# Optimization experiments

Measured on AMD Instinct MI355X. Metric: run time of the kernel, lower is better.

The kernel has to match this reference:

```python
import jax, jax.numpy as jnp
import numpy as np

EPS = 1e-8
NUM_HEADS = 8


def setup_inputs() -> dict:
    key = jax.random.key(0)
    ks = jax.random.split(key, 12)
    B, T, F = 8, 512, 512
    H = NUM_HEADS
    dh = F // H
    maxlen = 2048
    s = 0.02  # weight init scale
    inp = {
        "x": jax.random.normal(ks[0], (B, T, F), jnp.float32),
        "Wq": jax.random.normal(ks[1], (F, F), jnp.float32) * s,
        "bq": jax.random.normal(ks[2], (F,), jnp.float32) * s,
        "Wk": jax.random.normal(ks[3], (F, F), jnp.float32) * s,
        "bk": jax.random.normal(ks[4], (F,), jnp.float32) * s,
        "Wv": jax.random.normal(ks[5], (F, F), jnp.float32) * s,
        "bv": jax.random.normal(ks[6], (F,), jnp.float32) * s,
        "Wo": jax.random.normal(ks[7], (F, F), jnp.float32) * s,
        "bo": jax.random.normal(ks[8], (F,), jnp.float32) * s,
        "delta": jnp.ones((1,), jnp.float32),
        "cache_k": jax.random.normal(ks[9], (B * H, maxlen, dh), jnp.float32) * 0.1,
        "cache_v": jax.random.normal(ks[10], (B * H, maxlen, dh), jnp.float32) * 0.1,
    }
    return inp


def _split_heads(t, H):
    # torch.cat(torch.split(t, dh, dim=-1), dim=0): head index outermost on dim 0
    B, T, F = t.shape
    dh = F // H
    return t.reshape(B, T, H, dh).transpose(2, 0, 1, 3).reshape(H * B, T, dh)


def _merge_heads(t, H):
    HB, T, dh = t.shape
    B = HB // H
    return t.reshape(H, B, T, dh).transpose(1, 2, 0, 3).reshape(B, T, H * dh)


def reference(x, Wq, bq, Wk, bk, Wv, bv, Wo, bo, delta, cache_k, cache_v):
    B, T, F = x.shape
    H = NUM_HEADS
    maxlen = cache_k.shape[1]
    d = jnp.sqrt(jnp.asarray(F, jnp.float32))

    q = _split_heads(x @ Wq.T + bq, H)  # [H*B, T, dh]
    k = _split_heads(x @ Wk.T + bk, H)
    v = _split_heads(x @ Wv.T + bv, H)

    # rolling KV cache: drop oldest T, append new T -> length maxlen
    k_full = jnp.concatenate([cache_k[:, T:], k], axis=1)  # [H*B, maxlen, dh]
    v_full = jnp.concatenate([cache_v[:, T:], v], axis=1)

    # Gaussian positional bias G = exp(-(i-j)^2 / (delta^2 + EPS)), last T rows
    i = jnp.arange(maxlen, dtype=jnp.float32)
    ind = -(i[:, None] - i[None, :]) ** 2  # [maxlen, maxlen]
    G = jnp.exp(ind[-T:] / (delta[0] ** 2 + EPS))  # [T, maxlen]

    scores = jnp.abs(jnp.einsum('btd,bsd->bts', q, k_full) * G / d)
    attn = jax.nn.softmax(scores, axis=-1)  # [H*B, T, maxlen]
    o = jnp.einsum('bts,bsd->btd', attn, v_full)  # [H*B, T, dh]

    out = _merge_heads(o, H) @ Wo.T + bo  # [B, T, F]
    return out
```

## Files before the change

### kernel.cpp

```cpp
#include <hip/hip_runtime.h>
#include <cstdint>
#include <cstddef>


typedef _Float16 f16x8 __attribute__((ext_vector_type(8)));
typedef _Float16 f16x4 __attribute__((ext_vector_type(4)));
typedef float f32x4 __attribute__((ext_vector_type(4)));

#define GLOBAL_AS __attribute__((address_space(1)))
#define LDS_AS __attribute__((address_space(3)))

__launch_bounds__(256)
__global__ void prep(const float* __restrict__ x,
                     const float* __restrict__ Wq, const float* __restrict__ Wk,
                     const float* __restrict__ Wv, const float* __restrict__ Wo,
                     const float* __restrict__ cache_v,
                     _Float16* __restrict__ xh, _Float16* __restrict__ wh,
                     float* __restrict__ part, float* __restrict__ svnew) {
  const int bid = blockIdx.x;
  const int tid = threadIdx.x;
  if (bid < 2048) {
    long e = ((long)bid * 256 + tid) * 4;
    float4 v = *(const float4*)(x + e);
    f16x4 h;
    h[0] = (_Float16)v.x; h[1] = (_Float16)v.y;
    h[2] = (_Float16)v.z; h[3] = (_Float16)v.w;
    *(f16x4*)(xh + e) = h;
  } else if (bid < 3072) {
    long e = ((long)(bid - 2048) * 256 + tid) * 4;
    int seg = (int)(e >> 18);
    const float* w = seg == 0 ? Wq : seg == 1 ? Wk : seg == 2 ? Wv : Wo;
    float4 v = *(const float4*)(w + (e & 262143));
    f16x4 h;
    h[0] = (_Float16)v.x; h[1] = (_Float16)v.y;
    h[2] = (_Float16)v.z; h[3] = (_Float16)v.w;
    *(f16x4*)(wh + e) = h;
  } else if (bid < 4096) {
    int pb = bid - 3072;
    int hb = pb >> 4, chunk = pb & 15;
    int d = tid & 63, p = tid >> 6;
    int r0 = 512 + chunk * 96;
    float s = 0.f;
    for (int r = r0 + p; r < r0 + 96; r += 4)
      s += cache_v[((size_t)hb * 2048 + r) * 64 + d];
    __shared__ float red[256];
    red[tid] = s;
    __syncthreads();
    if (p == 0)
      part[(hb * 16 + chunk) * 64 + d] =
          red[d] + red[64 + d] + red[128 + d] + red[192 + d];
  } else {
    for (int i = tid; i < 4096; i += 256) svnew[i] = 0.f;
  }
}

__launch_bounds__(256)
__global__ void gemm_qkv(const _Float16* __restrict__ xh,
                         const _Float16* __restrict__ wh,
                         const float* __restrict__ bq,
                         const float* __restrict__ bk,
                         const float* __restrict__ bv,
                         _Float16* __restrict__ q, _Float16* __restrict__ k,
                         _Float16* __restrict__ v,
                         float* __restrict__ svnew) {
  __shared__ __align__(16) _Float16 As[2 * 128 * 32];
  __shared__ __align__(16) _Float16 Bs[2 * 64 * 32];
  const int tid = threadIdx.x;
  const int m0 = blockIdx.x * 128;
  const int n0g = blockIdx.y * 64;
  const int which = n0g >> 9;
  const int nloc0 = n0g & 511;
  const _Float16* Bsel = wh + (size_t)which * 262144;
  const float* bsel = which == 0 ? bq : which == 1 ? bk : bv;
  _Float16* osel = which == 0 ? q : which == 1 ? k : v;
  const int w = tid >> 6, lane = tid & 63;
  const int c16 = lane & 15, q4 = lane >> 4;
  const int wm = (w & 1) * 64, wn = (w >> 1) * 32;

  f32x4 acc[4][2];
#pragma unroll
  for (int i = 0; i < 4; i++)
#pragma unroll
    for (int j = 0; j < 2; j++) acc[i][j] = (f32x4){0.f, 0.f, 0.f, 0.f};

  for (int k0 = 0; k0 < 512; k0 += 64) {
    __syncthreads();
#pragma unroll
    for (int it = 0; it < 4; it++) {
      int c = it * 256 + tid;
      int sub = c >> 9, row = (c >> 2) & 127, c8 = (c & 3) * 8;
      __builtin_amdgcn_global_load_lds(
          (const GLOBAL_AS void*)(xh + (size_t)(m0 + row) * 512 + k0 + sub * 32 + c8),
          (LDS_AS void*)(As + c * 8), 16, 0, 0);
    }
#pragma unroll
    for (int it = 0; it < 2; it++) {
      int c = it * 256 + tid;
      int sub = c >> 8, row = (c >> 2) & 63, c8 = (c & 3) * 8;
      __builtin_amdgcn_global_load_lds(
          (const GLOBAL_AS void*)(Bsel + (size_t)(nloc0 + row) * 512 + k0 + sub * 32 + c8),
          (LDS_AS void*)(Bs + c * 8), 16, 0, 0);
    }
    __syncthreads();

#pragma unroll
    for (int sub = 0; sub < 2; sub++) {
      f16x8 af[4], bf[2];
#pragma unroll
      for (int i = 0; i < 4; i++)
        af[i] = *(const f16x8*)(As + sub * 4096 + (wm + i * 16 + c16) * 32 + q4 * 8);
#pragma unroll
      for (int j = 0; j < 2; j++)
        bf[j] = *(const f16x8*)(Bs + sub * 2048 + (wn + j * 16 + c16) * 32 + q4 * 8);
#pragma unroll
      for (int i = 0; i < 4; i++)
#pragma unroll
        for (int j = 0; j < 2; j++)
          acc[i][j] = __builtin_amdgcn_mfma_f32_16x16x32_f16(af[i], bf[j], acc[i][j], 0, 0, 0);
    }
  }

  const int mbase = m0 + wm + (q4 << 2);
  const int nbase = nloc0 + wn + c16;
  float cs[2] = {0.f, 0.f};
#pragma unroll
  for (int i = 0; i < 4; i++)
#pragma unroll
    for (int j = 0; j < 2; j++) {
      int fg = nbase + j * 16;
      float bv2 = bsel[fg];
      int h = fg >> 6, dd = fg & 63;
#pragma unroll
      for (int r = 0; r < 4; r++) {
        int m = mbase + i * 16 + r;
        int b = m >> 9, t = m & 511;
        float val = acc[i][j][r] + bv2;
        osel[(((size_t)((h << 3) + b) * 512 + t) << 6) + dd] = (_Float16)val;
        cs[j] += val;
      }
    }
  if (which == 2) {
    const int b = m0 >> 9;
#pragma unroll
    for (int j = 0; j < 2; j++) {
      cs[j] += __shfl_xor(cs[j], 16, 64);
      cs[j] += __shfl_xor(cs[j], 32, 64);
      if (q4 == 0) {
        int fg = nbase + j * 16;
        int h = fg >> 6, dd = fg & 63;
        atomicAdd(&svnew[((h << 3) + b) * 64 + dd], cs[j]);
      }
    }
  }
}

__launch_bounds__(256)
__global__ void attn_mfma(const _Float16* __restrict__ q,
                          const _Float16* __restrict__ k_new,
                          const _Float16* __restrict__ v_new,
                          const float* __restrict__ cache_k,
                          const float* __restrict__ cache_v,
                          const float* __restrict__ part,
                          const float* __restrict__ svnew,
                          const float* __restrict__ delta,
                          _Float16* __restrict__ o_merged) {
  const int hb = blockIdx.y;
  const int t0 = blockIdx.x * 64;
  const int jlo_t = 1520 + t0;

  __shared__ __align__(16) _Float16 Q_sh[64 * 72];
  __shared__ __align__(16) _Float16 K_sh[96 * 72];
  __shared__ __align__(16) _Float16 VT_sh[64 * 104];
  __shared__ __align__(16) _Float16 P_sh[64 * 104];
  __shared__ float G_sh[40];
  __shared__ float em_sh[64], id_sh[64], sv_sh[64];

  const int tid = threadIdx.x;
  const int w = tid >> 6, lane = tid & 63;
  const float dscale = 0.044194173824159216f;

  if (tid < 36) {
    int di = tid - 16;
    float inv_g = 1.0f / (delta[0] * delta[0] + 1e-8f);
    G_sh[tid] = (tid <= 32) ? expf(-(float)(di * di) * inv_g) : 0.f;
  }
  if (tid >= 64 && tid < 128) {
    int d = tid - 64;
    float s = svnew[hb * 64 + d];
#pragma unroll
    for (int c = 0; c < 16; c++) s += part[(hb * 16 + c) * 64 + d];
    sv_sh[d] = s;
  }
#pragma unroll
  for (int it = 0; it < 2; it++) {
    int idx = it * 256 + tid;
    int r = idx >> 3, c8 = (idx & 7) * 8;
    *(f16x8*)(Q_sh + r * 72 + c8) =
        *(const f16x8*)(q + ((size_t)hb * 512 + t0 + r) * 64 + c8);
  }
#pragma unroll
  for (int it = 0; it < 6; it++) {
    int idx = it * 256 + tid;
    int r = idx >> 4, c4 = idx & 15;
    int j = jlo_t + r;
    f16x4 kh, vh;
    if (j < 1536) {
      float4 k4 = *(const float4*)(cache_k + ((size_t)hb * 2048 + j + 512) * 64 + c4 * 4);
      float4 v4 = *(const float4*)(cache_v + ((size_t)hb * 2048 + j + 512) * 64 + c4 * 4);
      kh[0] = (_Float16)k4.x; kh[1] = (_Float16)k4.y;
      kh[2] = (_Float16)k4.z; kh[3] = (_Float16)k4.w;
      vh[0] = (_Float16)v4.x; vh[1] = (_Float16)v4.y;
      vh[2] = (_Float16)v4.z; vh[3] = (_Float16)v4.w;
    } else if (j < 2048) {
      kh = *(const f16x4*)(k_new + ((size_t)hb * 512 + (j - 1536)) * 64 + c4 * 4);
      vh = *(const f16x4*)(v_new + ((size_t)hb * 512 + (j - 1536)) * 64 + c4 * 4);
    } else {
#pragma unroll
      for (int e = 0; e < 4; e++) { kh[e] = (_Float16)0.f; vh[e] = (_Float16)0.f; }
    }
    *(f16x4*)(K_sh + r * 72 + c4 * 4) = kh;
#pragma unroll
    for (int e = 0; e < 4; e++) VT_sh[(c4 * 4 + e) * 104 + r] = vh[e];
  }
  __syncthreads();

  {
    const int c16 = lane & 15;
    const int q4 = lane >> 4;
    const int koff = q4 * 8;
    const int mrow = w * 16 + c16;
    f16x8 aq0 = *(const f16x8*)(Q_sh + mrow * 72 + koff);
    f16x8 aq1 = *(const f16x8*)(Q_sh + mrow * 72 + 32 + koff);
    f32x4 accS[6];
#pragma unroll
    for (int n = 0; n < 6; n++) accS[n] = (f32x4){0.f, 0.f, 0.f, 0.f};
#pragma unroll
    for (int n = 0; n < 6; n++) {
      f16x8 b0 = *(const f16x8*)(K_sh + (n * 16 + c16) * 72 + koff);
      f16x8 b1 = *(const f16x8*)(K_sh + (n * 16 + c16) * 72 + 32 + koff);
      accS[n] = __builtin_amdgcn_mfma_f32_16x16x32_f16(aq0, b0, accS[n], 0, 0, 0);
      accS[n] = __builtin_amdgcn_mfma_f32_16x16x32_f16(aq1, b1, accS[n], 0, 0, 0);
    }
    const int jmax = 527 - t0;
    float sc[6][4];
    float m_r[4] = {0.f, 0.f, 0.f, 0.f};
#pragma unroll
    for (int n = 0; n < 6; n++) {
      int jb = n * 16 + c16;
#pragma unroll
      for (int r = 0; r < 4; r++) {
        int row = w * 16 + q4 * 4 + r;
        int off = jb - row;
        bool valid = (off >= 0) && (off <= 32) && (jb <= jmax);
        int offc = min(max(off, 0), 32);
        float g = G_sh[offc];
        float val = valid ? fabsf(accS[n][r]) * dscale * g : 0.f;
        sc[n][r] = val;
        m_r[r] = fmaxf(m_r[r], val);
      }
    }
#pragma unroll
    for (int r = 0; r < 4; r++) {
#pragma unroll
      for (int mk = 1; mk < 16; mk <<= 1)
        m_r[r] = fmaxf(m_r[r], __shfl_xor(m_r[r], mk, 64));
    }
    float em_r[4], sum_r[4];
#pragma unroll
    for (int r = 0; r < 4; r++) { em_r[r] = expf(-m_r[r]); sum_r[r] = 0.f; }
#pragma unroll
    for (int n = 0; n < 6; n++) {
      int jb = n * 16 + c16;
#pragma unroll
      for (int r = 0; r < 4; r++) {
        int row = w * 16 + q4 * 4 + r;
        int off = jb - row;
        bool valid = (off >= 0) && (off <= 32) && (jb <= jmax);
        float wgt = valid ? (expf(sc[n][r] - m_r[r]) - em_r[r]) : 0.f;
        sum_r[r] += wgt;
        P_sh[row * 104 + jb] = (_Float16)wgt;
      }
    }
#pragma unroll
    for (int r = 0; r < 4; r++) {
#pragma unroll
      for (int mk = 1; mk < 16; mk <<= 1)
        sum_r[r] += __shfl_xor(sum_r[r], mk, 64);
      if (c16 == 0) {
        int row = w * 16 + q4 * 4 + r;
        em_sh[row] = em_r[r];
        id_sh[row] = 1.0f / (sum_r[r] + 2048.f * em_r[r]);
      }
    }
  }
  __syncthreads();

  f32x4 accO[4];
#pragma unroll
  for (int mi = 0; mi < 4; mi++) accO[mi] = (f32x4){0.f, 0.f, 0.f, 0.f};
  {
    const int koff = (lane >> 4) * 8;
    const int nrow = w * 16 + (lane & 15);
#pragma unroll
    for (int k = 0; k < 3; k++) {
      f16x8 bv = *(const f16x8*)(VT_sh + nrow * 104 + k * 32 + koff);
#pragma unroll
      for (int mi = 0; mi < 4; mi++) {
        f16x8 ap = *(const f16x8*)(P_sh + (mi * 16 + (lane & 15)) * 104 + k * 32 + koff);
        accO[mi] = __builtin_amdgcn_mfma_f32_16x16x32_f16(ap, bv, accO[mi], 0, 0, 0);
      }
    }
  }

  const int h = hb >> 3, b = hb & 7;
  const int d = w * 16 + (lane & 15);
  const float svd = sv_sh[d];
#pragma unroll
  for (int mi = 0; mi < 4; mi++)
#pragma unroll
    for (int r = 0; r < 4; r++) {
      int trow = mi * 16 + ((lane >> 4) << 2) + r;
      float val = (accO[mi][r] + em_sh[trow] * svd) * id_sh[trow];
      o_merged[((size_t)(b * 512 + t0 + trow)) * 512 + h * 64 + d] = (_Float16)val;
    }
}

__launch_bounds__(256)
__global__ void gemm_out(const _Float16* __restrict__ A,
                         const _Float16* __restrict__ Bw,
                         const float* __restrict__ bias,
                         float* __restrict__ out) {
  __shared__ __align__(16) _Float16 As[2 * 64 * 32];
  __shared__ __align__(16) _Float16 Bs[2 * 64 * 32];
  const int tid = threadIdx.x;
  const int m0 = blockIdx.x * 64;
  const int n0 = blockIdx.y * 64;
  const int w = tid >> 6, lane = tid & 63;
  const int c16 = lane & 15, q4 = lane >> 4;
  const int wm = (w & 1) * 32, wn = (w >> 1) * 32;

  f32x4 acc[2][2];
#pragma unroll
  for (int i = 0; i < 2; i++)
#pragma unroll
    for (int j = 0; j < 2; j++) acc[i][j] = (f32x4){0.f, 0.f, 0.f, 0.f};

  for (int k0 = 0; k0 < 512; k0 += 64) {
    __syncthreads();
#pragma unroll
    for (int it = 0; it < 2; it++) {
      int c = it * 256 + tid;
      int sub = c >> 8, row = (c >> 2) & 63, c8 = (c & 3) * 8;
      __builtin_amdgcn_global_load_lds(
          (const GLOBAL_AS void*)(A + (size_t)(m0 + row) * 512 + k0 + sub * 32 + c8),
          (LDS_AS void*)(As + c * 8), 16, 0, 0);
      __builtin_amdgcn_global_load_lds(
          (const GLOBAL_AS void*)(Bw + (size_t)(n0 + row) * 512 + k0 + sub * 32 + c8),
          (LDS_AS void*)(Bs + c * 8), 16, 0, 0);
    }
    __syncthreads();

#pragma unroll
    for (int sub = 0; sub < 2; sub++) {
      f16x8 af[2], bf[2];
#pragma unroll
      for (int i = 0; i < 2; i++)
        af[i] = *(const f16x8*)(As + sub * 2048 + (wm + i * 16 + c16) * 32 + q4 * 8);
#pragma unroll
      for (int j = 0; j < 2; j++)
        bf[j] = *(const f16x8*)(Bs + sub * 2048 + (wn + j * 16 + c16) * 32 + q4 * 8);
#pragma unroll
      for (int i = 0; i < 2; i++)
#pragma unroll
        for (int j = 0; j < 2; j++)
          acc[i][j] = __builtin_amdgcn_mfma_f32_16x16x32_f16(af[i], bf[j], acc[i][j], 0, 0, 0);
    }
  }

  const int mbase = m0 + wm + (q4 << 2);
  const int nbase = n0 + wn + c16;
#pragma unroll
  for (int i = 0; i < 2; i++)
#pragma unroll
    for (int j = 0; j < 2; j++) {
      int fg = nbase + j * 16;
      float bv = bias[fg];
#pragma unroll
      for (int r = 0; r < 4; r++) {
        int m = mbase + i * 16 + r;
        out[(size_t)m * 512 + fg] = acc[i][j][r] + bv;
      }
    }
}

extern "C" void kernel_launch(void* const* d_in, const int* in_sizes, int n_in,
                              void* d_out, int out_size, void* d_ws, size_t ws_size,
                              hipStream_t stream) {
  const float* x = (const float*)d_in[0];
  const float* Wq = (const float*)d_in[1];
  const float* bq = (const float*)d_in[2];
  const float* Wk = (const float*)d_in[3];
  const float* bk = (const float*)d_in[4];
  const float* Wv = (const float*)d_in[5];
  const float* bv = (const float*)d_in[6];
  const float* Wo = (const float*)d_in[7];
  const float* bo = (const float*)d_in[8];
  const float* delta = (const float*)d_in[9];
  const float* cache_k = (const float*)d_in[10];
  const float* cache_v = (const float*)d_in[11];
  float* out = (float*)d_out;

  _Float16* xh = (_Float16*)d_ws;
  _Float16* wh = xh + 2097152;
  _Float16* qf = wh + 1048576;
  _Float16* kf = qf + 2097152;
  _Float16* vf = kf + 2097152;
  float* part = (float*)(vf + 2097152);
  float* svnew = part + 65536;
  _Float16* oh = (_Float16*)(svnew + 4096);

  prep<<<4097, 256, 0, stream>>>(x, Wq, Wk, Wv, Wo, cache_v, xh, wh, part, svnew);

  dim3 g1(32, 24);
  gemm_qkv<<<g1, 256, 0, stream>>>(xh, wh, bq, bk, bv, qf, kf, vf, svnew);

  dim3 g2(8, 64);
  attn_mfma<<<g2, 256, 0, stream>>>(qf, kf, vf, cache_k, cache_v, part, svnew,
                                    delta, oh);

  dim3 g3(64, 8);
  gemm_out<<<g3, 256, 0, stream>>>(oh, wh + 3 * 262144, bo, out);
}
```

Before: 158.3 us.

## Vectorize cache_v partial sums, deepen GEMM K-tiles, swizzle blocks, raise MFMA priority

The prep kernel now sums cache_v rows with float4 loads and a 16-way LDS reduction instead of scalar loads. Both GEMMs load 128-wide K slices per stage, halving barrier round-trips at the cost of doubled LDS use. All three compute kernels remap block indices with an XCD-style swizzle to improve cache locality across chiplets. The attention MFMA loops are wrapped in s_setprio raises so the matrix-core work gets issue priority.

```diff
diff --git a/kernel.cpp b/kernel.cpp
--- a/kernel.cpp
+++ b/kernel.cpp
@@ -38,17 +38,28 @@
   } else if (bid < 4096) {
     int pb = bid - 3072;
     int hb = pb >> 4, chunk = pb & 15;
-    int d = tid & 63, p = tid >> 6;
+    int g = tid & 15, p = tid >> 4;
     int r0 = 512 + chunk * 96;
-    float s = 0.f;
-    for (int r = r0 + p; r < r0 + 96; r += 4)
-      s += cache_v[((size_t)hb * 2048 + r) * 64 + d];
-    __shared__ float red[256];
-    red[tid] = s;
+    float4 s4 = {0.f, 0.f, 0.f, 0.f};
+#pragma unroll
+    for (int it = 0; it < 6; it++) {
+      int r = r0 + p + it * 16;
+      float4 v = *(const float4*)(cache_v + ((size_t)hb * 2048 + r) * 64 + g * 4);
+      s4.x += v.x; s4.y += v.y; s4.z += v.z; s4.w += v.w;
+    }
+    __shared__ float4 red4[256];
+    red4[tid] = s4;
     __syncthreads();
-    if (p == 0)
-      part[(hb * 16 + chunk) * 64 + d] =
-          red[d] + red[64 + d] + red[128 + d] + red[192 + d];
+    if (tid < 64) {
+      int gg = tid >> 2, c = tid & 3;
+      float s = 0.f;
+#pragma unroll
+      for (int p2 = 0; p2 < 16; p2++) {
+        float4 v = red4[p2 * 16 + gg];
+        s += (c == 0) ? v.x : (c == 1) ? v.y : (c == 2) ? v.z : v.w;
+      }
+      part[(hb * 16 + chunk) * 64 + tid] = s;
+    }
   } else {
     for (int i = tid; i < 4096; i += 256) svnew[i] = 0.f;
   }
@@ -63,11 +74,15 @@
                          _Float16* __restrict__ q, _Float16* __restrict__ k,
                          _Float16* __restrict__ v,
                          float* __restrict__ svnew) {
-  __shared__ __align__(16) _Float16 As[2 * 128 * 32];
-  __shared__ __align__(16) _Float16 Bs[2 * 64 * 32];
+  __shared__ __align__(16) _Float16 As[4 * 128 * 32];
+  __shared__ __align__(16) _Float16 Bs[4 * 64 * 32];
   const int tid = threadIdx.x;
-  const int m0 = blockIdx.x * 128;
-  const int n0g = blockIdx.y * 64;
+  const int bid = blockIdx.x;
+  const int swz = (bid & 7) * 96 + (bid >> 3);
+  const int bx = swz / 24;
+  const int by = swz - bx * 24;
+  const int m0 = bx * 128;
+  const int n0g = by * 64;
   const int which = n0g >> 9;
   const int nloc0 = n0g & 511;
   const _Float16* Bsel = wh + (size_t)which * 262144;
@@ -83,10 +98,10 @@
 #pragma unroll
     for (int j = 0; j < 2; j++) acc[i][j] = (f32x4){0.f, 0.f, 0.f, 0.f};
 
-  for (int k0 = 0; k0 < 512; k0 += 64) {
+  for (int k0 = 0; k0 < 512; k0 += 128) {
     __syncthreads();
 #pragma unroll
-    for (int it = 0; it < 4; it++) {
+    for (int it = 0; it < 8; it++) {
       int c = it * 256 + tid;
       int sub = c >> 9, row = (c >> 2) & 127, c8 = (c & 3) * 8;
       __builtin_amdgcn_global_load_lds(
@@ -94,7 +109,7 @@
           (LDS_AS void*)(As + c * 8), 16, 0, 0);
     }
 #pragma unroll
-    for (int it = 0; it < 2; it++) {
+    for (int it = 0; it < 4; it++) {
       int c = it * 256 + tid;
       int sub = c >> 8, row = (c >> 2) & 63, c8 = (c & 3) * 8;
       __builtin_amdgcn_global_load_lds(
@@ -104,7 +119,7 @@
     __syncthreads();
 
 #pragma unroll
-    for (int sub = 0; sub < 2; sub++) {
+    for (int sub = 0; sub < 4; sub++) {
       f16x8 af[4], bf[2];
 #pragma unroll
       for (int i = 0; i < 4; i++)
@@ -164,8 +179,10 @@
                           const float* __restrict__ svnew,
                           const float* __restrict__ delta,
                           _Float16* __restrict__ o_merged) {
-  const int hb = blockIdx.y;
-  const int t0 = blockIdx.x * 64;
+  const int lin = blockIdx.y * 8 + blockIdx.x;
+  const int swz = (lin & 7) * 64 + (lin >> 3);
+  const int hb = swz >> 3;
+  const int t0 = (swz & 7) * 64;
   const int jlo_t = 1520 + t0;
 
   __shared__ __align__(16) _Float16 Q_sh[64 * 72];
@@ -234,6 +251,7 @@
     f32x4 accS[6];
 #pragma unroll
     for (int n = 0; n < 6; n++) accS[n] = (f32x4){0.f, 0.f, 0.f, 0.f};
+    __builtin_amdgcn_s_setprio(1);
 #pragma unroll
     for (int n = 0; n < 6; n++) {
       f16x8 b0 = *(const f16x8*)(K_sh + (n * 16 + c16) * 72 + koff);
@@ -241,6 +259,7 @@
       accS[n] = __builtin_amdgcn_mfma_f32_16x16x32_f16(aq0, b0, accS[n], 0, 0, 0);
       accS[n] = __builtin_amdgcn_mfma_f32_16x16x32_f16(aq1, b1, accS[n], 0, 0, 0);
     }
+    __builtin_amdgcn_s_setprio(0);
     const int jmax = 527 - t0;
     float sc[6][4];
     float m_r[4] = {0.f, 0.f, 0.f, 0.f};
@@ -301,6 +320,7 @@
   {
     const int koff = (lane >> 4) * 8;
     const int nrow = w * 16 + (lane & 15);
+    __builtin_amdgcn_s_setprio(1);
 #pragma unroll
     for (int k = 0; k < 3; k++) {
       f16x8 bv = *(const f16x8*)(VT_sh + nrow * 104 + k * 32 + koff);
@@ -310,6 +330,7 @@
         accO[mi] = __builtin_amdgcn_mfma_f32_16x16x32_f16(ap, bv, accO[mi], 0, 0, 0);
       }
     }
+    __builtin_amdgcn_s_setprio(0);
   }
 
   const int h = hb >> 3, b = hb & 7;
@@ -330,11 +351,13 @@
                          const _Float16* __restrict__ Bw,
                          const float* __restrict__ bias,
                          float* __restrict__ out) {
-  __shared__ __align__(16) _Float16 As[2 * 64 * 32];
-  __shared__ __align__(16) _Float16 Bs[2 * 64 * 32];
+  __shared__ __align__(16) _Float16 As[4 * 64 * 32];
+  __shared__ __align__(16) _Float16 Bs[4 * 64 * 32];
   const int tid = threadIdx.x;
-  const int m0 = blockIdx.x * 64;
-  const int n0 = blockIdx.y * 64;
+  const int bid = blockIdx.x;
+  const int swz = (bid & 7) * 64 + (bid >> 3);
+  const int m0 = (swz >> 3) * 64;
+  const int n0 = (swz & 7) * 64;
   const int w = tid >> 6, lane = tid & 63;
   const int c16 = lane & 15, q4 = lane >> 4;
   const int wm = (w & 1) * 32, wn = (w >> 1) * 32;
@@ -345,10 +368,10 @@
 #pragma unroll
     for (int j = 0; j < 2; j++) acc[i][j] = (f32x4){0.f, 0.f, 0.f, 0.f};
 
-  for (int k0 = 0; k0 < 512; k0 += 64) {
+  for (int k0 = 0; k0 < 512; k0 += 128) {
     __syncthreads();
 #pragma unroll
-    for (int it = 0; it < 2; it++) {
+    for (int it = 0; it < 4; it++) {
       int c = it * 256 + tid;
       int sub = c >> 8, row = (c >> 2) & 63, c8 = (c & 3) * 8;
       __builtin_amdgcn_global_load_lds(
@@ -361,7 +384,7 @@
     __syncthreads();
 
 #pragma unroll
-    for (int sub = 0; sub < 2; sub++) {
+    for (int sub = 0; sub < 4; sub++) {
       f16x8 af[2], bf[2];
 #pragma unroll
       for (int i = 0; i < 2; i++)
@@ -421,13 +444,11 @@
 
   prep<<<4097, 256, 0, stream>>>(x, Wq, Wk, Wv, Wo, cache_v, xh, wh, part, svnew);
 
-  dim3 g1(32, 24);
-  gemm_qkv<<<g1, 256, 0, stream>>>(xh, wh, bq, bk, bv, qf, kf, vf, svnew);
+  gemm_qkv<<<768, 256, 0, stream>>>(xh, wh, bq, bk, bv, qf, kf, vf, svnew);
 
   dim3 g2(8, 64);
   attn_mfma<<<g2, 256, 0, stream>>>(qf, kf, vf, cache_k, cache_v, part, svnew,
                                     delta, oh);
 
-  dim3 g3(64, 8);
-  gemm_out<<<g3, 256, 0, stream>>>(oh, wh + 3 * 262144, bo, out);
+  gemm_out<<<512, 256, 0, stream>>>(oh, wh + 3 * 262144, bo, out);
 }
```

After: 149.6 us. -5.5%, faster.
